# Performance work log

Hardware: AMD Instinct MI355X
Metric: run time of the kernel (lower is better)

Reference implementation:

```python
import jax, jax.numpy as jnp
import numpy as np

NUM_HEADS = 16
TEMPERATURE = 0.2


def setup_inputs() -> dict:
    key = jax.random.key(0)
    ks = jax.random.split(key, 6)
    B, TGT, SRC, D = 8, 256, 512, 1024
    seqs = jax.random.normal(ks[0], (B, TGT, D), jnp.float32)
    keys = jax.random.normal(ks[1], (B, SRC, D), jnp.float32)
    scale = 1.0 / np.sqrt(D).astype(np.float32)
    q_w = jax.random.normal(ks[2], (D, D), jnp.float32) * scale
    q_b = jax.random.normal(ks[3], (D,), jnp.float32) * 0.01
    k_w = jax.random.normal(ks[4], (D, D), jnp.float32) * scale
    k_b = jax.random.normal(ks[5], (D,), jnp.float32) * 0.01
    energy_bias = jnp.full((1,), -0.5, jnp.float32)
    return {"seqs": seqs, "keys": keys, "q_w": q_w, "q_b": q_b,
            "k_w": k_w, "k_b": k_b, "energy_bias": energy_bias}


def _monotonic_alignment(p):
    # p: (BH, tgt, src). Faithful to torch: T_i = triu(cumprod(1 - triu(roll(p_i),1)))
    # but T is built per target step inside a scan instead of materializing
    # the full (BH, tgt, src, src) tensor.
    BH, T, S = p.shape
    idx = jnp.arange(S)
    mask_strict = idx[None, :] > idx[:, None]   # triu(1)
    mask_ge = idx[None, :] >= idx[:, None]      # triu(0)
    p_roll = jnp.roll(p, 1, axis=-1)

    def step_T(pr_i):  # pr_i: (BH, S) -> (BH, S, S)
        pe = jnp.where(mask_strict, pr_i[:, None, :], 0.0)
        return jnp.where(mask_ge, jnp.cumprod(1.0 - pe, axis=-1), 0.0)

    T0 = step_T(p_roll[:, 0])
    alpha0 = p[:, 0] * T0[:, 0, :]              # (BH, S)

    def scan_fn(alpha, xs):
        p_i, pr_i = xs
        Ti = step_T(pr_i)                        # (BH, S, S)
        alpha_new = p_i * jnp.einsum('bm,bmn->bn', alpha, Ti)
        return alpha_new, alpha_new

    _, alphas = jax.lax.scan(
        scan_fn, alpha0,
        (jnp.swapaxes(p[:, 1:], 0, 1), jnp.swapaxes(p_roll[:, 1:], 0, 1)))
    return jnp.concatenate([alpha0[:, None], jnp.swapaxes(alphas, 0, 1)], axis=1)


def reference(seqs, keys, q_w, q_b, k_w, k_b, energy_bias):
    B, TGT, D = seqs.shape
    SRC = keys.shape[1]
    H = NUM_HEADS
    dh = D // H
    # EnergyProjection with num_layers=1: Linear + ReLU
    q = jax.nn.relu(seqs @ q_w.T + q_b)
    k = jax.nn.relu(keys @ k_w.T + k_b)
    q = q.reshape(B, TGT, H, dh).transpose(0, 2, 1, 3)   # (B,H,tgt,dh)
    k = k.reshape(B, SRC, H, dh).transpose(0, 2, 1, 3)   # (B,H,src,dh)
    energy = jnp.einsum('bhtd,bhsd->bhts', q, k) * (dh ** -0.5) + energy_bias[0]
    p_choose = jax.nn.sigmoid(energy / TEMPERATURE)       # (B,H,tgt,src)
    alpha = _monotonic_alignment(p_choose.reshape(B * H, TGT, SRC))
    alpha = alpha.reshape(B, H, TGT, SRC)
    return p_choose, alpha
```

## Files before the change

### kernel.cpp

```cpp
#include <hip/hip_runtime.h>

#define B_   8
#define TGT_ 256
#define SRC_ 512
#define D_   1024
#define H_   16
#define DH_  64

typedef _Float16 half4 __attribute__((ext_vector_type(4)));
typedef _Float16 half8 __attribute__((ext_vector_type(8)));
typedef float    floatx4 __attribute__((ext_vector_type(4)));

__device__ __forceinline__ void async_ld16(const void* g, void* l) {
    __builtin_amdgcn_global_load_lds(
        (const __attribute__((address_space(1))) void*)g,
        (__attribute__((address_space(3))) void*)l, 16, 0, 0);
}

template <int CTRL>
__device__ __forceinline__ float dppf(float x) {
    return __int_as_float(__builtin_amdgcn_update_dpp(
        0, __float_as_int(x), CTRL, 0xF, 0xF, true));
}
__device__ __forceinline__ float rdlane(float x, int lane) {
    return __int_as_float(__builtin_amdgcn_readlane(__float_as_int(x), lane));
}

__global__ __launch_bounds__(256) void cvt_kernel(
    const float* __restrict__ s0, const float* __restrict__ s1,
    const float* __restrict__ s2, const float* __restrict__ s3,
    _Float16* __restrict__ d0, _Float16* __restrict__ d1,
    _Float16* __restrict__ d2, _Float16* __restrict__ d3)
{
    const int bid = blockIdx.x;
    const float* src; _Float16* dst; int base;
    if      (bid < 2048) { src = s0; dst = d0; base = bid;        }
    else if (bid < 6144) { src = s1; dst = d1; base = bid - 2048; }
    else if (bid < 7168) { src = s2; dst = d2; base = bid - 6144; }
    else                 { src = s3; dst = d3; base = bid - 7168; }
    const int idx = (base * 256 + threadIdx.x) * 4;
    float4 v = *(const float4*)(src + idx);
    half4 o = { (_Float16)v.x, (_Float16)v.y, (_Float16)v.z, (_Float16)v.w };
    *(half4*)(dst + idx) = o;
}

__global__ __launch_bounds__(256, 2) void proj_mfma_kernel(
    const _Float16* __restrict__ seqs_h, const _Float16* __restrict__ keys_h,
    const _Float16* __restrict__ qw_h,   const _Float16* __restrict__ kw_h,
    const float* __restrict__ q_b,       const float* __restrict__ k_b,
    _Float16* __restrict__ Qh, _Float16* __restrict__ Kh)
{
    __shared__ __align__(16) _Float16 As[128 * 32];
    __shared__ __align__(16) _Float16 Ws[128 * 32];

    const int tid = threadIdx.x;
    const int bx  = blockIdx.x;
    const int K   = D_, N = D_;

    const _Float16* A; const _Float16* W; const float* bias; _Float16* C;
    int bm0;
    if (bx < 16) { A = seqs_h; W = qw_h; bias = q_b; C = Qh; bm0 = bx * 128; }
    else         { A = keys_h; W = kw_h; bias = k_b; C = Kh; bm0 = (bx - 16) * 128; }
    const int bn0 = blockIdx.y * 128;

    const int c0 = tid, c1 = tid + 256;
    const _Float16* gA0 = A + (size_t)(bm0 + (c0 >> 2)) * K + (c0 & 3) * 8;
    const _Float16* gA1 = A + (size_t)(bm0 + (c1 >> 2)) * K + (c1 & 3) * 8;
    const _Float16* gW0 = W + (size_t)(bn0 + (c0 >> 2)) * K + (c0 & 3) * 8;
    const _Float16* gW1 = W + (size_t)(bn0 + (c1 >> 2)) * K + (c1 & 3) * 8;
    _Float16* lA0 = As + c0 * 8;
    _Float16* lA1 = As + c1 * 8;
    _Float16* lW0 = Ws + c0 * 8;
    _Float16* lW1 = Ws + c1 * 8;

    floatx4 acc[4][4];
#pragma unroll
    for (int i = 0; i < 4; ++i)
#pragma unroll
        for (int j = 0; j < 4; ++j) acc[i][j] = (floatx4){0.f, 0.f, 0.f, 0.f};

    const int lane = tid & 63;
    const int wid  = tid >> 6;
    const int wm   = (wid >> 1) * 64;
    const int wn   = (wid & 1) * 64;
    const int fm   = lane & 15;
    const int fk   = (lane >> 4) * 8;
    const _Float16* aF = As + (wm + fm) * 32 + fk;
    const _Float16* bF = Ws + (wn + fm) * 32 + fk;

    for (int k0 = 0; k0 < K; k0 += 32) {
        __syncthreads();
        async_ld16(gA0 + k0, lA0);
        async_ld16(gA1 + k0, lA1);
        async_ld16(gW0 + k0, lW0);
        async_ld16(gW1 + k0, lW1);
        __syncthreads();

        half8 a[4], b[4];
#pragma unroll
        for (int i = 0; i < 4; ++i) {
            a[i] = *(const half8*)(aF + i * 16 * 32);
            b[i] = *(const half8*)(bF + i * 16 * 32);
        }
#pragma unroll
        for (int mt = 0; mt < 4; ++mt)
#pragma unroll
            for (int nt = 0; nt < 4; ++nt)
                acc[mt][nt] = __builtin_amdgcn_mfma_f32_16x16x32_f16(
                    a[mt], b[nt], acc[mt][nt], 0, 0, 0);
    }

    const int er = (lane >> 4) * 4;
#pragma unroll
    for (int nt = 0; nt < 4; ++nt) {
        const int col = bn0 + wn + nt * 16 + fm;
        const float bv = bias[col];
#pragma unroll
        for (int mt = 0; mt < 4; ++mt) {
            const int row0 = bm0 + wm + mt * 16 + er;
#pragma unroll
            for (int r = 0; r < 4; ++r) {
                float v = acc[mt][nt][r] + bv;
                v = fmaxf(v, 0.0f);
                C[(size_t)(row0 + r) * N + col] = (_Float16)v;
            }
        }
    }
}

__global__ __launch_bounds__(256, 4) void energy_mfma_kernel(
    const _Float16* __restrict__ Q, const _Float16* __restrict__ K,
    const float* __restrict__ eb_ptr, float* __restrict__ P)
{
    __shared__ __align__(16) unsigned char smem[64 * 132 * 4];
    _Float16* Qt = (_Float16*)smem;
    _Float16* Kt = Qt + 2 * 64 * 32;
    float*    pT = (float*)smem;

    const int tid = threadIdx.x;
    const int bh  = blockIdx.x;
    const int b   = bh >> 4;
    const int h   = bh & 15;
    const int t0  = blockIdx.y << 6;
    const int s0  = blockIdx.z << 7;

#pragma unroll
    for (int u = 0; u < 2; ++u) {
        const int unit = tid + u * 256;
        const int row = unit >> 3, hc = unit & 7;
        half8 v = *(const half8*)(Q + ((size_t)(b * TGT_ + t0 + row)) * D_ + h * DH_ + hc * 8);
        *(half8*)(Qt + (hc >> 2) * (64 * 32) + row * 32 + (hc & 3) * 8) = v;
    }
#pragma unroll
    for (int u = 0; u < 4; ++u) {
        const int unit = tid + u * 256;
        const int row = unit >> 3, hc = unit & 7;
        half8 v = *(const half8*)(K + ((size_t)(b * SRC_ + s0 + row)) * D_ + h * DH_ + hc * 8);
        *(half8*)(Kt + (hc >> 2) * (128 * 32) + row * 32 + (hc & 3) * 8) = v;
    }
    __syncthreads();

    const int lane = tid & 63;
    const int wid  = tid >> 6;
    const int wm   = (wid >> 1) * 32;
    const int wn   = (wid & 1) * 64;
    const int fm   = lane & 15;
    const int fk   = (lane >> 4) * 8;

    floatx4 acc[2][4];
#pragma unroll
    for (int i = 0; i < 2; ++i)
#pragma unroll
        for (int j = 0; j < 4; ++j) acc[i][j] = (floatx4){0.f, 0.f, 0.f, 0.f};

#pragma unroll
    for (int ks = 0; ks < 2; ++ks) {
        const _Float16* aB = Qt + ks * (64 * 32) + (wm + fm) * 32 + fk;
        const _Float16* bB = Kt + ks * (128 * 32) + (wn + fm) * 32 + fk;
        half8 a0 = *(const half8*)(aB);
        half8 a1 = *(const half8*)(aB + 16 * 32);
        half8 b0 = *(const half8*)(bB);
        half8 b1 = *(const half8*)(bB + 16 * 32);
        half8 b2 = *(const half8*)(bB + 32 * 32);
        half8 b3 = *(const half8*)(bB + 48 * 32);
        acc[0][0] = __builtin_amdgcn_mfma_f32_16x16x32_f16(a0, b0, acc[0][0], 0, 0, 0);
        acc[0][1] = __builtin_amdgcn_mfma_f32_16x16x32_f16(a0, b1, acc[0][1], 0, 0, 0);
        acc[0][2] = __builtin_amdgcn_mfma_f32_16x16x32_f16(a0, b2, acc[0][2], 0, 0, 0);
        acc[0][3] = __builtin_amdgcn_mfma_f32_16x16x32_f16(a0, b3, acc[0][3], 0, 0, 0);
        acc[1][0] = __builtin_amdgcn_mfma_f32_16x16x32_f16(a1, b0, acc[1][0], 0, 0, 0);
        acc[1][1] = __builtin_amdgcn_mfma_f32_16x16x32_f16(a1, b1, acc[1][1], 0, 0, 0);
        acc[1][2] = __builtin_amdgcn_mfma_f32_16x16x32_f16(a1, b2, acc[1][2], 0, 0, 0);
        acc[1][3] = __builtin_amdgcn_mfma_f32_16x16x32_f16(a1, b3, acc[1][3], 0, 0, 0);
    }

    __syncthreads();

    const float eb = eb_ptr[0];
    const int er = (lane >> 4) * 4;
#pragma unroll
    for (int mt = 0; mt < 2; ++mt) {
#pragma unroll
        for (int nt = 0; nt < 4; ++nt) {
            const int s_b = wn + nt * 16 + fm;
#pragma unroll
            for (int r = 0; r < 4; ++r) {
                const int t_b = wm + mt * 16 + er + r;
                float x = (acc[mt][nt][r] * 0.125f + eb) * 5.0f;
                float p = 1.0f / (1.0f + __expf(-x));
                pT[t_b * 132 + s_b] = p;
            }
        }
    }
    __syncthreads();

#pragma unroll
    for (int u0 = 0; u0 < 8; ++u0) {
        const int u = tid + u0 * 256;
        const int row = u >> 5, c = u & 31;
        float4 v = *(const float4*)&pT[row * 132 + c * 4];
        *(float4*)&P[((size_t)bh * TGT_ + t0 + row) * SRC_ + s0 + c * 4] = v;
    }
}

__global__ __launch_bounds__(64, 1) void align_kernel(
    const float* __restrict__ P, float* __restrict__ Alpha)
{
    const int bh   = blockIdx.x;
    const int lane = threadIdx.x;
    const float* prow = P + (size_t)bh * TGT_ * SRC_;
    float* arow       = Alpha + (size_t)bh * TGT_ * SRC_;
    const int n0 = lane << 3;

    float bprev[8];
#pragma unroll
    for (int j = 0; j < 8; ++j) bprev[j] = 0.0f;
    if (lane == 0) bprev[0] = 1.0f;

    float4 bufA[8], bufB[8];
#pragma unroll
    for (int j = 0; j < 8; ++j) {
        const float* r = prow + (size_t)j * SRC_ + n0;
        bufA[j] = *(const float4*)r;
        bufB[j] = *(const float4*)(r + 4);
    }

    for (int g = 0; g < TGT_ / 8; ++g) {
#pragma unroll
        for (int jj = 0; jj < 8; ++jj) {
            const int i = g * 8 + jj;
            float4 ca = bufA[jj], cb = bufB[jj];
            if (i + 8 < TGT_) {
                const float* r = prow + (size_t)(i + 8) * SRC_ + n0;
                bufA[jj] = *(const float4*)r;
                bufB[jj] = *(const float4*)(r + 4);
            }
            float pl[8] = {ca.x, ca.y, ca.z, ca.w, cb.x, cb.y, cb.z, cb.w};

            float pm1 = dppf<0x111>(pl[7]);
            {
                float r15 = rdlane(pl[7], 15);
                float r31 = rdlane(pl[7], 31);
                float r47 = rdlane(pl[7], 47);
                pm1 = (lane == 16) ? r15 : pm1;
                pm1 = (lane == 32) ? r31 : pm1;
                pm1 = (lane == 48) ? r47 : pm1;
            }
            float a[8];
            a[0] = (lane == 0) ? 0.0f : (1.0f - pm1);
#pragma unroll
            for (int j = 1; j < 8; ++j) a[j] = 1.0f - pl[j - 1];

            float Aj[8], Bj[8];
            float A = a[0], Bv = bprev[0];
            Aj[0] = A; Bj[0] = Bv;
#pragma unroll
            for (int j = 1; j < 8; ++j) {
                Bv = fmaf(a[j], Bv, bprev[j]);
                A  = a[j] * A;
                Aj[j] = A; Bj[j] = Bv;
            }

            float As_ = A, Bs = Bv;
            {
                float Ash, Bsh;
                Ash = dppf<0x111>(As_); Bsh = dppf<0x111>(Bs);
                Ash = ((lane & 15) >= 1) ? Ash : 1.0f;
                Bs  = fmaf(As_, Bsh, Bs); As_ = As_ * Ash;
                Ash = dppf<0x112>(As_); Bsh = dppf<0x112>(Bs);
                Ash = ((lane & 15) >= 2) ? Ash : 1.0f;
                Bs  = fmaf(As_, Bsh, Bs); As_ = As_ * Ash;
                Ash = dppf<0x114>(As_); Bsh = dppf<0x114>(Bs);
                Ash = ((lane & 15) >= 4) ? Ash : 1.0f;
                Bs  = fmaf(As_, Bsh, Bs); As_ = As_ * Ash;
                Ash = dppf<0x118>(As_); Bsh = dppf<0x118>(Bs);
                Ash = ((lane & 15) >= 8) ? Ash : 1.0f;
                Bs  = fmaf(As_, Bsh, Bs); As_ = As_ * Ash;
            }

            float PB;
            {
                float B15 = rdlane(Bs, 15);
                float A31 = rdlane(As_, 31), B31 = rdlane(Bs, 31);
                float B47 = rdlane(Bs, 47);
                float PB1 = B15;
                float PB2 = fmaf(A31, PB1, B31);
                float PB3 = fmaf(rdlane(As_, 47), PB2, B47);
                const int seg = lane >> 4;
                PB = (seg == 0) ? 0.0f : ((seg == 1) ? PB1 : ((seg == 2) ? PB2 : PB3));
            }

            float EA = dppf<0x111>(As_);
            float EB = dppf<0x111>(Bs);
            EA = (lane & 15) ? EA : 1.0f;
            float cin = fmaf(EA, PB, EB);

            float an[8];
#pragma unroll
            for (int j = 0; j < 8; ++j) {
                float c = fmaf(Aj[j], cin, Bj[j]);
                an[j] = pl[j] * c;
                bprev[j] = an[j];
            }
            float4 o0 = {an[0], an[1], an[2], an[3]};
            float4 o1 = {an[4], an[5], an[6], an[7]};
            float* dst = arow + (size_t)i * SRC_ + n0;
            *(float4*)dst       = o0;
            *(float4*)(dst + 4) = o1;
        }
    }
}

extern "C" void kernel_launch(void* const* d_in, const int* in_sizes, int n_in,
                              void* d_out, int out_size, void* d_ws, size_t ws_size,
                              hipStream_t stream) {
    const float* seqs = (const float*)d_in[0];
    const float* keys = (const float*)d_in[1];
    const float* q_w  = (const float*)d_in[2];
    const float* q_b  = (const float*)d_in[3];
    const float* k_w  = (const float*)d_in[4];
    const float* k_b  = (const float*)d_in[5];
    const float* eb   = (const float*)d_in[6];

    float* out   = (float*)d_out;
    float* P     = out;
    float* Alpha = out + (size_t)B_ * H_ * TGT_ * SRC_;

    _Float16* Qh     = (_Float16*)d_ws;
    _Float16* Kh     = Qh + (size_t)B_ * TGT_ * D_;
    _Float16* seqs_h = Kh + (size_t)B_ * SRC_ * D_;
    _Float16* keys_h = seqs_h + (size_t)B_ * TGT_ * D_;
    _Float16* qw_h   = keys_h + (size_t)B_ * SRC_ * D_;
    _Float16* kw_h   = qw_h + (size_t)D_ * D_;

    cvt_kernel<<<dim3(8192), 256, 0, stream>>>(seqs, keys, q_w, k_w,
                                               seqs_h, keys_h, qw_h, kw_h);
    {
        dim3 grid(48, D_ / 128);
        proj_mfma_kernel<<<grid, 256, 0, stream>>>(seqs_h, keys_h, qw_h, kw_h,
                                                   q_b, k_b, Qh, Kh);
    }
    {
        dim3 grid(B_ * H_, TGT_ / 64, SRC_ / 128);
        energy_mfma_kernel<<<grid, 256, 0, stream>>>(Qh, Kh, eb, P);
    }
    align_kernel<<<dim3(B_ * H_), 64, 0, stream>>>(P, Alpha);
}
```

Before: 232.3 us.

## Fuse energy GEMM into alignment scan with producer/consumer warps per head

Merges the energy MFMA kernel and the alignment scan into one kernel per batch-head. Four producer waves compute 16-row tiles of sigmoid energies into a double-buffered shared-memory buffer, while one consumer wave runs the monotonic scan and writes both P and alpha. This removes the global write and re-read of P between kernels and one launch. In exchange the energy GEMM now runs on only 128 blocks, and every tile is gated by a block-wide barrier that couples the producers to the serial scan.

```diff
diff --git a/kernel.cpp b/kernel.cpp
--- a/kernel.cpp
+++ b/kernel.cpp
@@ -128,107 +128,36 @@
     }
 }
 
-__global__ __launch_bounds__(256, 4) void energy_mfma_kernel(
+__global__ __launch_bounds__(320, 1) void energy_align_kernel(
     const _Float16* __restrict__ Q, const _Float16* __restrict__ K,
-    const float* __restrict__ eb_ptr, float* __restrict__ P)
+    const float* __restrict__ eb_ptr, float* __restrict__ P,
+    float* __restrict__ Alpha)
 {
-    __shared__ __align__(16) unsigned char smem[64 * 132 * 4];
-    _Float16* Qt = (_Float16*)smem;
-    _Float16* Kt = Qt + 2 * 64 * 32;
-    float*    pT = (float*)smem;
-
-    const int tid = threadIdx.x;
-    const int bh  = blockIdx.x;
-    const int b   = bh >> 4;
-    const int h   = bh & 15;
-    const int t0  = blockIdx.y << 6;
-    const int s0  = blockIdx.z << 7;
-
-#pragma unroll
-    for (int u = 0; u < 2; ++u) {
-        const int unit = tid + u * 256;
-        const int row = unit >> 3, hc = unit & 7;
-        half8 v = *(const half8*)(Q + ((size_t)(b * TGT_ + t0 + row)) * D_ + h * DH_ + hc * 8);
-        *(half8*)(Qt + (hc >> 2) * (64 * 32) + row * 32 + (hc & 3) * 8) = v;
-    }
-#pragma unroll
-    for (int u = 0; u < 4; ++u) {
-        const int unit = tid + u * 256;
-        const int row = unit >> 3, hc = unit & 7;
-        half8 v = *(const half8*)(K + ((size_t)(b * SRC_ + s0 + row)) * D_ + h * DH_ + hc * 8);
-        *(half8*)(Kt + (hc >> 2) * (128 * 32) + row * 32 + (hc & 3) * 8) = v;
-    }
-    __syncthreads();
-
+    __shared__ __align__(16) _Float16 Kt[2 * 512 * 32];
+    __shared__ __align__(16) float    Pb[2][16][512];
+
+    const int tid  = threadIdx.x;
+    const int bh   = blockIdx.x;
+    const int b    = bh >> 4;
+    const int h    = bh & 15;
     const int lane = tid & 63;
     const int wid  = tid >> 6;
-    const int wm   = (wid >> 1) * 32;
-    const int wn   = (wid & 1) * 64;
-    const int fm   = lane & 15;
-    const int fk   = (lane >> 4) * 8;
-
-    floatx4 acc[2][4];
-#pragma unroll
-    for (int i = 0; i < 2; ++i)
-#pragma unroll
-        for (int j = 0; j < 4; ++j) acc[i][j] = (floatx4){0.f, 0.f, 0.f, 0.f};
-
-#pragma unroll
-    for (int ks = 0; ks < 2; ++ks) {
-        const _Float16* aB = Qt + ks * (64 * 32) + (wm + fm) * 32 + fk;
-        const _Float16* bB = Kt + ks * (128 * 32) + (wn + fm) * 32 + fk;
-        half8 a0 = *(const half8*)(aB);
-        half8 a1 = *(const half8*)(aB + 16 * 32);
-        half8 b0 = *(const half8*)(bB);
-        half8 b1 = *(const half8*)(bB + 16 * 32);
-        half8 b2 = *(const half8*)(bB + 32 * 32);
-        half8 b3 = *(const half8*)(bB + 48 * 32);
-        acc[0][0] = __builtin_amdgcn_mfma_f32_16x16x32_f16(a0, b0, acc[0][0], 0, 0, 0);
-        acc[0][1] = __builtin_amdgcn_mfma_f32_16x16x32_f16(a0, b1, acc[0][1], 0, 0, 0);
-        acc[0][2] = __builtin_amdgcn_mfma_f32_16x16x32_f16(a0, b2, acc[0][2], 0, 0, 0);
-        acc[0][3] = __builtin_amdgcn_mfma_f32_16x16x32_f16(a0, b3, acc[0][3], 0, 0, 0);
-        acc[1][0] = __builtin_amdgcn_mfma_f32_16x16x32_f16(a1, b0, acc[1][0], 0, 0, 0);
-        acc[1][1] = __builtin_amdgcn_mfma_f32_16x16x32_f16(a1, b1, acc[1][1], 0, 0, 0);
-        acc[1][2] = __builtin_amdgcn_mfma_f32_16x16x32_f16(a1, b2, acc[1][2], 0, 0, 0);
-        acc[1][3] = __builtin_amdgcn_mfma_f32_16x16x32_f16(a1, b3, acc[1][3], 0, 0, 0);
-    }
-
-    __syncthreads();
+
+    for (int u = tid; u < 4096; u += 320) {
+        const int row = u >> 3, hc = u & 7;
+        half8 v = *(const half8*)(K + ((size_t)(b * SRC_ + row)) * D_ + h * DH_ + hc * 8);
+        *(half8*)(Kt + (hc >> 2) * (512 * 32) + row * 32 + (hc & 3) * 8) = v;
+    }
 
     const float eb = eb_ptr[0];
-    const int er = (lane >> 4) * 4;
-#pragma unroll
-    for (int mt = 0; mt < 2; ++mt) {
-#pragma unroll
-        for (int nt = 0; nt < 4; ++nt) {
-            const int s_b = wn + nt * 16 + fm;
-#pragma unroll
-            for (int r = 0; r < 4; ++r) {
-                const int t_b = wm + mt * 16 + er + r;
-                float x = (acc[mt][nt][r] * 0.125f + eb) * 5.0f;
-                float p = 1.0f / (1.0f + __expf(-x));
-                pT[t_b * 132 + s_b] = p;
-            }
-        }
-    }
-    __syncthreads();
-
-#pragma unroll
-    for (int u0 = 0; u0 < 8; ++u0) {
-        const int u = tid + u0 * 256;
-        const int row = u >> 5, c = u & 31;
-        float4 v = *(const float4*)&pT[row * 132 + c * 4];
-        *(float4*)&P[((size_t)bh * TGT_ + t0 + row) * SRC_ + s0 + c * 4] = v;
-    }
-}
-
-__global__ __launch_bounds__(64, 1) void align_kernel(
-    const float* __restrict__ P, float* __restrict__ Alpha)
-{
-    const int bh   = blockIdx.x;
-    const int lane = threadIdx.x;
-    const float* prow = P + (size_t)bh * TGT_ * SRC_;
-    float* arow       = Alpha + (size_t)bh * TGT_ * SRC_;
+    const int fm  = lane & 15;
+    const int fk  = (lane >> 4) * 8;
+    const int er  = (lane >> 4) * 4;
+    const int s0w = (wid > 0) ? (wid - 1) * 128 : 0;
+    const _Float16* qbase = Q + ((size_t)(b * TGT_) + fm) * D_ + h * DH_ + fk;
+
+    float* Pg = P     + (size_t)bh * TGT_ * SRC_;
+    float* Ag = Alpha + (size_t)bh * TGT_ * SRC_;
     const int n0 = lane << 3;
 
     float bprev[8];
@@ -236,97 +165,132 @@
     for (int j = 0; j < 8; ++j) bprev[j] = 0.0f;
     if (lane == 0) bprev[0] = 1.0f;
 
-    float4 bufA[8], bufB[8];
-#pragma unroll
-    for (int j = 0; j < 8; ++j) {
-        const float* r = prow + (size_t)j * SRC_ + n0;
-        bufA[j] = *(const float4*)r;
-        bufB[j] = *(const float4*)(r + 4);
-    }
-
-    for (int g = 0; g < TGT_ / 8; ++g) {
-#pragma unroll
-        for (int jj = 0; jj < 8; ++jj) {
-            const int i = g * 8 + jj;
-            float4 ca = bufA[jj], cb = bufB[jj];
-            if (i + 8 < TGT_) {
-                const float* r = prow + (size_t)(i + 8) * SRC_ + n0;
-                bufA[jj] = *(const float4*)r;
-                bufB[jj] = *(const float4*)(r + 4);
+    auto produce = [&](int tile, int nb) {
+        const _Float16* qp = qbase + (size_t)(tile * 16) * D_;
+        half8 a0 = *(const half8*)(qp);
+        half8 a1 = *(const half8*)(qp + 32);
+        floatx4 acc[8];
+#pragma unroll
+        for (int nt = 0; nt < 8; ++nt) acc[nt] = (floatx4){0.f, 0.f, 0.f, 0.f};
+        const _Float16* bB = Kt + (s0w + fm) * 32 + fk;
+#pragma unroll
+        for (int nt = 0; nt < 8; ++nt) {
+            half8 b0 = *(const half8*)(bB + nt * (16 * 32));
+            half8 b1 = *(const half8*)(bB + 512 * 32 + nt * (16 * 32));
+            acc[nt] = __builtin_amdgcn_mfma_f32_16x16x32_f16(a0, b0, acc[nt], 0, 0, 0);
+            acc[nt] = __builtin_amdgcn_mfma_f32_16x16x32_f16(a1, b1, acc[nt], 0, 0, 0);
+        }
+#pragma unroll
+        for (int nt = 0; nt < 8; ++nt) {
+            const int s = s0w + nt * 16 + fm;
+#pragma unroll
+            for (int r = 0; r < 4; ++r) {
+                float x = (acc[nt][r] * 0.125f + eb) * 5.0f;
+                Pb[nb][er + r][s] = 1.0f / (1.0f + __expf(-x));
             }
-            float pl[8] = {ca.x, ca.y, ca.z, ca.w, cb.x, cb.y, cb.z, cb.w};
-
-            float pm1 = dppf<0x111>(pl[7]);
-            {
-                float r15 = rdlane(pl[7], 15);
-                float r31 = rdlane(pl[7], 31);
-                float r47 = rdlane(pl[7], 47);
-                pm1 = (lane == 16) ? r15 : pm1;
-                pm1 = (lane == 32) ? r31 : pm1;
-                pm1 = (lane == 48) ? r47 : pm1;
+        }
+    };
+
+    __syncthreads();
+
+    if (wid > 0) produce(0, 0);
+    __syncthreads();
+
+    for (int tile = 0; tile < 16; ++tile) {
+        const int nb = tile & 1;
+        if (wid > 0) {
+            if (tile + 1 < 16) produce(tile + 1, nb ^ 1);
+        } else {
+            float4 ca = *(const float4*)&Pb[nb][0][n0];
+            float4 cb = *(const float4*)&Pb[nb][0][n0 + 4];
+            for (int jj = 0; jj < 16; ++jj) {
+                float4 na = ca, nv = cb;
+                if (jj < 15) {
+                    na = *(const float4*)&Pb[nb][jj + 1][n0];
+                    nv = *(const float4*)&Pb[nb][jj + 1][n0 + 4];
+                }
+                float pl[8] = {ca.x, ca.y, ca.z, ca.w, cb.x, cb.y, cb.z, cb.w};
+
+                float pm1 = dppf<0x111>(pl[7]);
+                {
+                    float r15 = rdlane(pl[7], 15);
+                    float r31 = rdlane(pl[7], 31);
+                    float r47 = rdlane(pl[7], 47);
+                    pm1 = (lane == 16) ? r15 : pm1;
+                    pm1 = (lane == 32) ? r31 : pm1;
+                    pm1 = (lane == 48) ? r47 : pm1;
+                }
+                float a[8];
+                a[0] = (lane == 0) ? 0.0f : (1.0f - pm1);
+#pragma unroll
+                for (int j = 1; j < 8; ++j) a[j] = 1.0f - pl[j - 1];
+
+                float Aj[8], Bj[8];
+                float A = a[0], Bv = bprev[0];
+                Aj[0] = A; Bj[0] = Bv;
+#pragma unroll
+                for (int j = 1; j < 8; ++j) {
+                    Bv = fmaf(a[j], Bv, bprev[j]);
+                    A  = a[j] * A;
+                    Aj[j] = A; Bj[j] = Bv;
+                }
+
+                float As_ = A, Bs = Bv;
+                {
+                    float Ash, Bsh;
+                    Ash = dppf<0x111>(As_); Bsh = dppf<0x111>(Bs);
+                    Ash = ((lane & 15) >= 1) ? Ash : 1.0f;
+                    Bs  = fmaf(As_, Bsh, Bs); As_ = As_ * Ash;
+                    Ash = dppf<0x112>(As_); Bsh = dppf<0x112>(Bs);
+                    Ash = ((lane & 15) >= 2) ? Ash : 1.0f;
+                    Bs  = fmaf(As_, Bsh, Bs); As_ = As_ * Ash;
+                    Ash = dppf<0x114>(As_); Bsh = dppf<0x114>(Bs);
+                    Ash = ((lane & 15) >= 4) ? Ash : 1.0f;
+                    Bs  = fmaf(As_, Bsh, Bs); As_ = As_ * Ash;
+                    Ash = dppf<0x118>(As_); Bsh = dppf<0x118>(Bs);
+                    Ash = ((lane & 15) >= 8) ? Ash : 1.0f;
+                    Bs  = fmaf(As_, Bsh, Bs); As_ = As_ * Ash;
+                }
+
+                float PB;
+                {
+                    float B15 = rdlane(Bs, 15);
+                    float A31 = rdlane(As_, 31), B31 = rdlane(Bs, 31);
+                    float B47 = rdlane(Bs, 47);
+                    float PB1 = B15;
+                    float PB2 = fmaf(A31, PB1, B31);
+                    float PB3 = fmaf(rdlane(As_, 47), PB2, B47);
+                    const int seg = lane >> 4;
+                    PB = (seg == 0) ? 0.0f : ((seg == 1) ? PB1 : ((seg == 2) ? PB2 : PB3));
+                }
+
+                float EA = dppf<0x111>(As_);
+                float EB = dppf<0x111>(Bs);
+                EA = (lane & 15) ? EA : 1.0f;
+                float cin = fmaf(EA, PB, EB);
+
+                float an[8];
+#pragma unroll
+                for (int j = 0; j < 8; ++j) {
+                    float c = fmaf(Aj[j], cin, Bj[j]);
+                    an[j] = pl[j] * c;
+                    bprev[j] = an[j];
+                }
+
+                const int t = tile * 16 + jj;
+                float* pg = Pg + (size_t)t * SRC_ + n0;
+                *(float4*)pg       = ca;
+                *(float4*)(pg + 4) = cb;
+                float4 o0 = {an[0], an[1], an[2], an[3]};
+                float4 o1 = {an[4], an[5], an[6], an[7]};
+                float* ag = Ag + (size_t)t * SRC_ + n0;
+                *(float4*)ag       = o0;
+                *(float4*)(ag + 4) = o1;
+
+                ca = na; cb = nv;
             }
-            float a[8];
-            a[0] = (lane == 0) ? 0.0f : (1.0f - pm1);
-#pragma unroll
-            for (int j = 1; j < 8; ++j) a[j] = 1.0f - pl[j - 1];
-
-            float Aj[8], Bj[8];
-            float A = a[0], Bv = bprev[0];
-            Aj[0] = A; Bj[0] = Bv;
-#pragma unroll
-            for (int j = 1; j < 8; ++j) {
-                Bv = fmaf(a[j], Bv, bprev[j]);
-                A  = a[j] * A;
-                Aj[j] = A; Bj[j] = Bv;
-            }
-
-            float As_ = A, Bs = Bv;
-            {
-                float Ash, Bsh;
-                Ash = dppf<0x111>(As_); Bsh = dppf<0x111>(Bs);
-                Ash = ((lane & 15) >= 1) ? Ash : 1.0f;
-                Bs  = fmaf(As_, Bsh, Bs); As_ = As_ * Ash;
-                Ash = dppf<0x112>(As_); Bsh = dppf<0x112>(Bs);
-                Ash = ((lane & 15) >= 2) ? Ash : 1.0f;
-                Bs  = fmaf(As_, Bsh, Bs); As_ = As_ * Ash;
-                Ash = dppf<0x114>(As_); Bsh = dppf<0x114>(Bs);
-                Ash = ((lane & 15) >= 4) ? Ash : 1.0f;
-                Bs  = fmaf(As_, Bsh, Bs); As_ = As_ * Ash;
-                Ash = dppf<0x118>(As_); Bsh = dppf<0x118>(Bs);
-                Ash = ((lane & 15) >= 8) ? Ash : 1.0f;
-                Bs  = fmaf(As_, Bsh, Bs); As_ = As_ * Ash;
-            }
-
-            float PB;
-            {
-                float B15 = rdlane(Bs, 15);
-                float A31 = rdlane(As_, 31), B31 = rdlane(Bs, 31);
-                float B47 = rdlane(Bs, 47);
-                float PB1 = B15;
-                float PB2 = fmaf(A31, PB1, B31);
-                float PB3 = fmaf(rdlane(As_, 47), PB2, B47);
-                const int seg = lane >> 4;
-                PB = (seg == 0) ? 0.0f : ((seg == 1) ? PB1 : ((seg == 2) ? PB2 : PB3));
-            }
-
-            float EA = dppf<0x111>(As_);
-            float EB = dppf<0x111>(Bs);
-            EA = (lane & 15) ? EA : 1.0f;
-            float cin = fmaf(EA, PB, EB);
-
-            float an[8];
-#pragma unroll
-            for (int j = 0; j < 8; ++j) {
-                float c = fmaf(Aj[j], cin, Bj[j]);
-                an[j] = pl[j] * c;
-                bprev[j] = an[j];
-            }
-            float4 o0 = {an[0], an[1], an[2], an[3]};
-            float4 o1 = {an[4], an[5], an[6], an[7]};
-            float* dst = arow + (size_t)i * SRC_ + n0;
-            *(float4*)dst       = o0;
-            *(float4*)(dst + 4) = o1;
-        }
+        }
+        __syncthreads();
     }
 }
 
@@ -359,9 +323,5 @@
         proj_mfma_kernel<<<grid, 256, 0, stream>>>(seqs_h, keys_h, qw_h, kw_h,
                                                    q_b, k_b, Qh, Kh);
     }
-    {
-        dim3 grid(B_ * H_, TGT_ / 64, SRC_ / 128);
-        energy_mfma_kernel<<<grid, 256, 0, stream>>>(Qh, Kh, eb, P);
-    }
-    align_kernel<<<dim3(B_ * H_), 64, 0, stream>>>(P, Alpha);
-}
+    energy_align_kernel<<<dim3(B_ * H_), 320, 0, stream>>>(Qh, Kh, eb, P, Alpha);
+}
```

New measurement: 235.7 us. About the same (+1.5%).
